# Optimization experiments

Measured on AMD Instinct MI355X. Metric: run time of the kernel, lower is better.

Reference implementation:

```python
import jax, jax.numpy as jnp
import numpy as np

K_SIZE = 3
STRIDE = 1
PAD = 1


def _extract_patches(X, k, stride, pad):
    """X: [N,H,W,C] -> patches [N,Ho,Wo,k*k*C], ordered (dh, dw, c) to match
    filters.reshape(c_out, k*k*C)."""
    Xp = jnp.pad(X, ((0, 0), (pad, pad), (pad, pad), (0, 0)))
    N, Hp, Wp, C = Xp.shape
    Ho = (Hp - k) // stride + 1
    Wo = (Wp - k) // stride + 1
    slabs = [Xp[:, dh:dh + stride * Ho:stride, dw:dw + stride * Wo:stride, :]
             for dh in range(k) for dw in range(k)]  # fixed small k*k loop
    P = jnp.stack(slabs, axis=3)  # [N,Ho,Wo,k*k,C]
    return P.reshape(N, Ho, Wo, k * k * C)


def setup_inputs() -> dict:
    key = jax.random.key(0)
    k1, k2 = jax.random.split(key)
    X = jax.random.normal(k1, (8, 32, 32, 32), dtype=jnp.float32)
    filters = jax.random.normal(k2, (64, 3, 3, 32), dtype=jnp.float32)
    return {"X": X, "filters": filters}


def reference(X, filters):
    # AdderNet forward: Z[n,h,w,f] = sum_{dh,dw,c} |window(n,h,w) - filters[f]|
    c_out = filters.shape[0]
    P = _extract_patches(X, K_SIZE, STRIDE, PAD)  # [N,Ho,Wo,K]
    N, Ho, Wo, K = P.shape
    F = filters.reshape(c_out, K)
    # L1 distance between every patch and every filter: [M, c_out]
    D = jnp.abs(P.reshape(-1, 1, K) - F[None, :, :]).sum(axis=-1)
    return D.reshape(N, Ho, Wo, c_out)
```

## Files before the change

### kernel.cpp

```cpp
#include <hip/hip_runtime.h>


#define BLOCK 256

__global__ __launch_bounds__(256, 2) void adder_fwd(const float* __restrict__ X,
                                                    const float* __restrict__ Fg,
                                                    float* __restrict__ out) {
    __shared__ float Xs[3 * 34 * 36];
    __shared__ float Fs[32 * 288];

    const int b = blockIdx.x;
    const int fhalf = b & 1;
    const int h = (b >> 1) & 31;
    const int n = b >> 6;
    const int tid = threadIdx.x;

    {
        const float4* src = (const float4*)(Fg + (size_t)fhalf * (32 * 288));
        float4* dst = (float4*)Fs;
        #pragma unroll
        for (int i = 0; i < 9; ++i) dst[tid + BLOCK * i] = src[tid + BLOCK * i];
    }

    {
        #pragma unroll
        for (int i = 0; i < 4; ++i) {
            int idx = tid + BLOCK * i;
            if (idx < 816) {
                int c4 = idx & 7;
                int t  = idx >> 3;
                int wc = t % 34;
                int r  = t / 34;
                int hr = h + r - 1;
                int w  = wc - 1;
                float4 v = make_float4(0.f, 0.f, 0.f, 0.f);
                if ((unsigned)hr < 32u && (unsigned)w < 32u) {
                    v = ((const float4*)(X + (((size_t)n * 32 + hr) * 32 + w) * 32))[c4];
                }
                ((float4*)(Xs + (r * 34 + wc) * 36))[c4] = v;
            }
        }
    }
    __syncthreads();

    const int w  = tid & 31;
    const int fg = tid >> 5;

    float4 a0 = make_float4(0.f, 0.f, 0.f, 0.f);
    float4 a1 = make_float4(0.f, 0.f, 0.f, 0.f);
    float4 a2 = make_float4(0.f, 0.f, 0.f, 0.f);
    float4 a3 = make_float4(0.f, 0.f, 0.f, 0.f);

    #pragma unroll
    for (int r = 0; r < 3; ++r) {
        #pragma unroll
        for (int dw = 0; dw < 3; ++dw) {
            const float4* xp = (const float4*)(Xs + (r * 34 + w + dw) * 36);
            const float*  fb = Fs + (fg * 4) * 288 + (r * 3 + dw) * 32;
            #pragma unroll
            for (int c4 = 0; c4 < 8; ++c4) {
                float4 xv = xp[c4];
                float4 f0 = ((const float4*)(fb + 0 * 288))[c4];
                float4 f1 = ((const float4*)(fb + 1 * 288))[c4];
                float4 f2 = ((const float4*)(fb + 2 * 288))[c4];
                float4 f3 = ((const float4*)(fb + 3 * 288))[c4];
                a0.x += fabsf(xv.x - f0.x); a0.y += fabsf(xv.y - f0.y);
                a0.z += fabsf(xv.z - f0.z); a0.w += fabsf(xv.w - f0.w);
                a1.x += fabsf(xv.x - f1.x); a1.y += fabsf(xv.y - f1.y);
                a1.z += fabsf(xv.z - f1.z); a1.w += fabsf(xv.w - f1.w);
                a2.x += fabsf(xv.x - f2.x); a2.y += fabsf(xv.y - f2.y);
                a2.z += fabsf(xv.z - f2.z); a2.w += fabsf(xv.w - f2.w);
                a3.x += fabsf(xv.x - f3.x); a3.y += fabsf(xv.y - f3.y);
                a3.z += fabsf(xv.z - f3.z); a3.w += fabsf(xv.w - f3.w);
            }
        }
    }

    float4 res;
    res.x = (a0.x + a0.y) + (a0.z + a0.w);
    res.y = (a1.x + a1.y) + (a1.z + a1.w);
    res.z = (a2.x + a2.y) + (a2.z + a2.w);
    res.w = (a3.x + a3.y) + (a3.z + a3.w);

    float4* o4 = (float4*)out;
    o4[(((size_t)n * 32 + h) * 32 + w) * 16 + fhalf * 8 + fg] = res;
}

extern "C" void kernel_launch(void* const* d_in, const int* in_sizes, int n_in,
                              void* d_out, int out_size, void* d_ws, size_t ws_size,
                              hipStream_t stream) {
    const float* X = (const float*)d_in[0];
    const float* F = (const float*)d_in[1];
    float* out = (float*)d_out;
    adder_fwd<<<dim3(512), dim3(256), 0, stream>>>(X, F, out);
}
```

Measured before the change: 71.86 us.

## Read filters from global via wave-uniform scalar loads and tile two output rows

Removes the shared-memory filter staging and instead has each wave read its four filters straight from global memory through a readfirstlane-uniform index, so the compiler can issue scalar loads. Each block now handles two output rows and a quarter of the filters, staging four padded input rows. This frees about 36KB of LDS per block and cuts LDS traffic, with the uniform filter reads going through the scalar cache. The trade is many more small global filter loads per block and scalar accumulators that form longer serial add chains.

```diff
diff --git a/kernel.cpp b/kernel.cpp
--- a/kernel.cpp
+++ b/kernel.cpp
@@ -6,84 +6,71 @@
 __global__ __launch_bounds__(256, 2) void adder_fwd(const float* __restrict__ X,
                                                     const float* __restrict__ Fg,
                                                     float* __restrict__ out) {
-    __shared__ float Xs[3 * 34 * 36];
-    __shared__ float Fs[32 * 288];
+    __shared__ float Xs[4 * 34 * 36];
 
     const int b = blockIdx.x;
-    const int fhalf = b & 1;
-    const int h = (b >> 1) & 31;
+    const int fq = b & 3;
+    const int hp = (b >> 2) & 15;
     const int n = b >> 6;
+    const int h0 = hp * 2;
     const int tid = threadIdx.x;
 
-    {
-        const float4* src = (const float4*)(Fg + (size_t)fhalf * (32 * 288));
-        float4* dst = (float4*)Fs;
-        #pragma unroll
-        for (int i = 0; i < 9; ++i) dst[tid + BLOCK * i] = src[tid + BLOCK * i];
-    }
-
-    {
-        #pragma unroll
-        for (int i = 0; i < 4; ++i) {
-            int idx = tid + BLOCK * i;
-            if (idx < 816) {
-                int c4 = idx & 7;
-                int t  = idx >> 3;
-                int wc = t % 34;
-                int r  = t / 34;
-                int hr = h + r - 1;
-                int w  = wc - 1;
-                float4 v = make_float4(0.f, 0.f, 0.f, 0.f);
-                if ((unsigned)hr < 32u && (unsigned)w < 32u) {
-                    v = ((const float4*)(X + (((size_t)n * 32 + hr) * 32 + w) * 32))[c4];
-                }
-                ((float4*)(Xs + (r * 34 + wc) * 36))[c4] = v;
+    #pragma unroll
+    for (int i = 0; i < 5; ++i) {
+        int idx = tid + BLOCK * i;
+        if (idx < 1088) {
+            int c4 = idx & 7;
+            int t  = idx >> 3;
+            int wc = t % 34;
+            int rr = t / 34;
+            int hr = h0 + rr - 1;
+            int gw = wc - 1;
+            float4 v = make_float4(0.f, 0.f, 0.f, 0.f);
+            if ((unsigned)hr < 32u && (unsigned)gw < 32u) {
+                v = ((const float4*)(X + (((size_t)n * 32 + hr) * 32 + gw) * 32))[c4];
             }
+            ((float4*)(Xs + (rr * 34 + wc) * 36))[c4] = v;
         }
     }
     __syncthreads();
 
-    const int w  = tid & 31;
-    const int fg = tid >> 5;
+    const int w    = tid & 31;
+    const int hh   = (tid >> 5) & 1;
+    const int wave = __builtin_amdgcn_readfirstlane(tid >> 6);
+    const int f0   = fq * 16 + wave * 4;
 
-    float4 a0 = make_float4(0.f, 0.f, 0.f, 0.f);
-    float4 a1 = make_float4(0.f, 0.f, 0.f, 0.f);
-    float4 a2 = make_float4(0.f, 0.f, 0.f, 0.f);
-    float4 a3 = make_float4(0.f, 0.f, 0.f, 0.f);
+    const float* fb = Fg + (size_t)f0 * 288;
+
+    float a0 = 0.f, a1 = 0.f, a2 = 0.f, a3 = 0.f;
 
     #pragma unroll
     for (int r = 0; r < 3; ++r) {
         #pragma unroll
         for (int dw = 0; dw < 3; ++dw) {
-            const float4* xp = (const float4*)(Xs + (r * 34 + w + dw) * 36);
-            const float*  fb = Fs + (fg * 4) * 288 + (r * 3 + dw) * 32;
+            const float4* xp = (const float4*)(Xs + ((hh + r) * 34 + (w + dw)) * 36);
+            const float*  ftap = fb + (r * 3 + dw) * 32;
             #pragma unroll
             for (int c4 = 0; c4 < 8; ++c4) {
                 float4 xv = xp[c4];
-                float4 f0 = ((const float4*)(fb + 0 * 288))[c4];
-                float4 f1 = ((const float4*)(fb + 1 * 288))[c4];
-                float4 f2 = ((const float4*)(fb + 2 * 288))[c4];
-                float4 f3 = ((const float4*)(fb + 3 * 288))[c4];
-                a0.x += fabsf(xv.x - f0.x); a0.y += fabsf(xv.y - f0.y);
-                a0.z += fabsf(xv.z - f0.z); a0.w += fabsf(xv.w - f0.w);
-                a1.x += fabsf(xv.x - f1.x); a1.y += fabsf(xv.y - f1.y);
-                a1.z += fabsf(xv.z - f1.z); a1.w += fabsf(xv.w - f1.w);
-                a2.x += fabsf(xv.x - f2.x); a2.y += fabsf(xv.y - f2.y);
-                a2.z += fabsf(xv.z - f2.z); a2.w += fabsf(xv.w - f2.w);
-                a3.x += fabsf(xv.x - f3.x); a3.y += fabsf(xv.y - f3.y);
-                a3.z += fabsf(xv.z - f3.z); a3.w += fabsf(xv.w - f3.w);
+                float4 f0v = ((const float4*)(ftap + 0 * 288))[c4];
+                float4 f1v = ((const float4*)(ftap + 1 * 288))[c4];
+                float4 f2v = ((const float4*)(ftap + 2 * 288))[c4];
+                float4 f3v = ((const float4*)(ftap + 3 * 288))[c4];
+                a0 += fabsf(xv.x - f0v.x) + fabsf(xv.y - f0v.y)
+                    + fabsf(xv.z - f0v.z) + fabsf(xv.w - f0v.w);
+                a1 += fabsf(xv.x - f1v.x) + fabsf(xv.y - f1v.y)
+                    + fabsf(xv.z - f1v.z) + fabsf(xv.w - f1v.w);
+                a2 += fabsf(xv.x - f2v.x) + fabsf(xv.y - f2v.y)
+                    + fabsf(xv.z - f2v.z) + fabsf(xv.w - f2v.w);
+                a3 += fabsf(xv.x - f3v.x) + fabsf(xv.y - f3v.y)
+                    + fabsf(xv.z - f3v.z) + fabsf(xv.w - f3v.w);
             }
         }
     }
 
-    float4 res;
-    res.x = (a0.x + a0.y) + (a0.z + a0.w);
-    res.y = (a1.x + a1.y) + (a1.z + a1.w);
-    res.z = (a2.x + a2.y) + (a2.z + a2.w);
-    res.w = (a3.x + a3.y) + (a3.z + a3.w);
-
     float4* o4 = (float4*)out;
-    o4[(((size_t)n * 32 + h) * 32 + w) * 16 + fhalf * 8 + fg] = res;
+    o4[(((size_t)n * 32 + h0 + hh) * 32 + w) * 16 + (f0 >> 2)] =
+        make_float4(a0, a1, a2, a3);
 }
 
 extern "C" void kernel_launch(void* const* d_in, const int* in_sizes, int n_in,
```

Result: faster. 69.45 us (-3.4%).
